# Optimization experiments

Hardware: AMD Instinct MI355X
Metric: run time of the kernel (lower is better)

## Reference

```python
import jax, jax.numpy as jnp
import numpy as np

NUM_HEADS = 32
HEAD_DIM = 32  # hard-coded in the module


def _rope_sincos(seq_len, head_dim):
    # NOTE: module uses arange(0, head_dim)/head_dim (full dim, not the usual /2 stride)
    inv_freq = 1.0 / (10000.0 ** (jnp.arange(0, head_dim, dtype=jnp.float32) / head_dim))
    freqs = jnp.outer(jnp.arange(seq_len, dtype=jnp.float32), inv_freq)  # [S, D]
    # original repeats over heads then reshapes -> identical values per head,
    # so broadcasting with shape [1, S, 1, D] is equivalent.
    return jnp.sin(freqs)[None, :, None, :], jnp.cos(freqs)[None, :, None, :]


def _apply_rope(x, sin, cos):
    x1, x2 = jnp.split(x, 2, axis=-1)
    x_rot = jnp.concatenate([-x2, x1], axis=-1)
    return x * cos + x_rot * sin


def setup_inputs() -> dict:
    key = jax.random.key(0)
    B, S, H, D = 2, 2048, NUM_HEADS, HEAD_DIM
    dm = H * D
    k1, k2 = jax.random.split(key)
    x = jax.random.normal(k1, (B, S, dm), dtype=jnp.float32)
    W_qkv = jax.random.normal(k2, (dm, 3 * dm), dtype=jnp.float32) / np.sqrt(dm).astype(np.float32)
    mask = jnp.tril(jnp.ones((S, S), dtype=bool))[None, None]  # causal, [1,1,S,S]
    return {"x": x, "W_qkv": W_qkv, "mask": mask}


def reference(x, W_qkv, mask):
    B, S, dm = x.shape
    H, D = NUM_HEADS, HEAD_DIM
    qkv = x @ W_qkv  # [B, S, 3*H*D], no bias
    q, k, v = jnp.split(qkv, 3, axis=-1)
    q = q.reshape(B, S, H, D)
    k = k.reshape(B, S, H, D)
    v = v.reshape(B, S, H, D)

    sin, cos = _rope_sincos(S, D)
    q = _apply_rope(q, sin, cos)
    k = _apply_rope(k, sin, cos)

    # [B, H, S, D]
    q = q.transpose(0, 2, 1, 3)
    k = k.transpose(0, 2, 1, 3)
    v = v.transpose(0, 2, 1, 3)

    scale = 1.0 / np.sqrt(D).astype(np.float32)
    attn = jnp.einsum('bhqd,bhkd->bhqk', q, k) * scale  # [B, H, S, S]
    attn = jnp.where(mask, attn, jnp.float32(-jnp.inf))
    attn = jax.nn.softmax(attn, axis=-1)
    out = jnp.einsum('bhqk,bhkd->bhqd', attn, v)  # [B, H, S, D]
    return out.transpose(0, 2, 1, 3).reshape(B, S, H * D)
```

## Files before the change

kernel.cpp:

```cpp
#include <hip/hip_runtime.h>
#include <cstdint>
#include <cstddef>

#define BB 2
#define SS 2048
#define HH 32
#define DD 32
#define DM 1024
#define MROWS 4096
#define NQKV 3072

#define QSCALE 0.25503486f

typedef __attribute__((ext_vector_type(8))) short bf16x8;
typedef __attribute__((ext_vector_type(4))) float f32x4;
typedef __attribute__((address_space(1))) unsigned int gu32;
typedef __attribute__((address_space(3))) unsigned int lu32;

__device__ __forceinline__ unsigned short f2bf(float f) {
    union { float f; unsigned int u; } v;
    v.f = f;
    unsigned int u = v.u;
    u += 0x7fffu + ((u >> 16) & 1u);
    return (unsigned short)(u >> 16);
}

__device__ __forceinline__ unsigned int cvt_pk_bf16(float a, float b) {
    unsigned int r;
    asm("v_cvt_pk_bf16_f32 %0, %1, %2" : "=v"(r) : "v"(a), "v"(b));
    return r;
}

__global__ void conv_x_k(const float* __restrict__ x, unsigned short* __restrict__ xb, int n4) {
    int i = blockIdx.x * 256 + threadIdx.x;
    if (i < n4) {
        float4 v = ((const float4*)x)[i];
        ushort4 o;
        o.x = f2bf(v.x); o.y = f2bf(v.y); o.z = f2bf(v.z); o.w = f2bf(v.w);
        ((ushort4*)xb)[i] = o;
    }
}

__global__ void conv_wT_k(const float* __restrict__ w, unsigned short* __restrict__ wT) {
    __shared__ unsigned short tile[64][65];
    const int n0 = blockIdx.x * 64;
    const int k0 = blockIdx.y * 64;
    const int tx = threadIdx.x & 63;
    const int ty = threadIdx.x >> 6;
    for (int i = ty; i < 64; i += 4)
        tile[i][tx] = f2bf(w[(size_t)(k0 + i) * NQKV + n0 + tx]);
    __syncthreads();
    for (int i = ty; i < 64; i += 4)
        wT[(size_t)(n0 + i) * 1024 + k0 + tx] = tile[tx][i];
}

__global__ void rope_tab_k(float* __restrict__ st, float* __restrict__ ct) {
    int i = blockIdx.x * 256 + threadIdx.x;
    int s = i >> 5, d = i & 31;
    float inv = exp2f((float)d * -0.41524101186092029f);
    float f = (float)s * inv;
    float sv, cv;
    sincosf(f, &sv, &cv);
    st[i] = sv;
    ct[i] = cv;
}

__global__ __launch_bounds__(256) void qkv_gemm_k(
        const unsigned short* __restrict__ xb,
        const unsigned short* __restrict__ wTp,
        const float* __restrict__ st, const float* __restrict__ ct,
        unsigned short* __restrict__ qbuf,
        unsigned short* __restrict__ kbuf,
        unsigned short* __restrict__ vtbuf) {
    __shared__ unsigned short smem[2 * 128 * 32];
    unsigned short* As = smem;
    unsigned short* Bs = smem + 4096;
    const int m0 = blockIdx.x * 128;
    const int n0 = blockIdx.y * 128;
    const int tid = threadIdx.x;
    const int w = tid >> 6, lane = tid & 63;
    const int quad = lane >> 4, l16 = lane & 15;
    const int wr = w >> 1, wc = w & 1;

    f32x4 acc[4][4];
#pragma unroll
    for (int i = 0; i < 4; ++i)
#pragma unroll
        for (int j = 0; j < 4; ++j)
            acc[i][j] = (f32x4){0.f, 0.f, 0.f, 0.f};

    const int Ra = lane >> 2;
    const int ca = lane & 3;

    for (int k0 = 0; k0 < 1024; k0 += 32) {
        __syncthreads();
#pragma unroll
        for (int q = 0; q < 2; ++q) {
            const int seg = w * 2 + q;
            const int row = seg * 16 + Ra;
            const unsigned short* ga = xb  + (size_t)(m0 + row) * 1024 + k0 + ca * 8;
            const unsigned short* gb = wTp + (size_t)(n0 + row) * 1024 + k0 + ca * 8;
            __builtin_amdgcn_global_load_lds((gu32*)ga, (lu32*)(As + seg * 512), 16, 0, 0);
            __builtin_amdgcn_global_load_lds((gu32*)gb, (lu32*)(Bs + seg * 512), 16, 0, 0);
        }
        __syncthreads();
        bf16x8 af[4], bfv[4];
#pragma unroll
        for (int i = 0; i < 4; ++i)
            af[i] = *(const bf16x8*)(As + (wr * 64 + i * 16 + l16) * 32 + quad * 8);
#pragma unroll
        for (int j = 0; j < 4; ++j)
            bfv[j] = *(const bf16x8*)(Bs + (wc * 64 + j * 16 + l16) * 32 + quad * 8);
#pragma unroll
        for (int i = 0; i < 4; ++i)
#pragma unroll
            for (int j = 0; j < 4; ++j)
                acc[i][j] = __builtin_amdgcn_mfma_f32_16x16x32_bf16(af[i], bfv[j], acc[i][j], 0, 0, 0);
    }

    const int sec = n0 >> 10;
    const int rowb = m0 + wr * 64;
    const int colb = n0 + wc * 64;
    if (sec < 2) {
        unsigned short* dst = (sec == 0) ? qbuf : kbuf;
        const float qs = (sec == 0) ? QSCALE : 1.0f;
        const int d1 = l16, d2 = l16 + 16;
#pragma unroll
        for (int jp = 0; jp < 2; ++jp) {
            const int col1 = colb + jp * 32 + l16;
            const int h = (col1 & 1023) >> 5;
#pragma unroll
            for (int i = 0; i < 4; ++i) {
#pragma unroll
                for (int r = 0; r < 4; ++r) {
                    const int row = rowb + i * 16 + quad * 4 + r;
                    const int bb = row >> 11;
                    const int s = row & 2047;
                    const float x1 = acc[i][jp * 2][r];
                    const float x2 = acc[i][jp * 2 + 1][r];
                    const float sn1 = st[s * 32 + d1] * qs, cs1 = ct[s * 32 + d1] * qs;
                    const float sn2 = st[s * 32 + d2] * qs, cs2 = ct[s * 32 + d2] * qs;
                    unsigned short o1 = f2bf(x1 * cs1 - x2 * sn1);
                    unsigned short o2 = f2bf(x2 * cs2 + x1 * sn2);
                    unsigned short* p = dst + (size_t)((bb * 32 + h) * 2048 + s) * 32;
                    p[d1] = o1;
                    p[d2] = o2;
                }
            }
        }
    } else {
        __syncthreads();
        unsigned short* tw = smem + w * 2048;
        const int bbi = rowb >> 11;
        const int srow = rowb & 2047;
        const int colB = colb - 2048;
#pragma unroll
        for (int j = 0; j < 4; ++j) {
#pragma unroll
            for (int i = 0; i < 4; ++i) {
                uint2 pk;
                pk.x = cvt_pk_bf16(acc[i][j][0], acc[i][j][1]);
                pk.y = cvt_pk_bf16(acc[i][j][2], acc[i][j][3]);
                *(uint2*)&tw[l16 * 66 + i * 16 + quad * 4] = pk;
            }
#pragma unroll
            for (int c = 0; c < 16; ++c) {
                const int col = colB + j * 16 + c;
                const int hh = col >> 5, d = col & 31;
                vtbuf[((size_t)(bbi * 32 + hh) * 32 + d) * 2048 + srow + lane] = tw[c * 66 + lane];
            }
        }
    }
}

__global__ __launch_bounds__(256) void attn_k(
        const unsigned short* __restrict__ qb,
        const unsigned short* __restrict__ kb,
        const unsigned short* __restrict__ vt,
        float* __restrict__ out) {
    __shared__ unsigned short Pl[4][2][32][40];
    const int tid = threadIdx.x;
    const int w = tid >> 6, lane = tid & 63;
    const int quad = lane >> 4, l16 = lane & 15;
    const int bh = blockIdx.x >> 3;
    const int pr = blockIdx.x & 7;
    const int b = bh >> 5, h = bh & 31;

    const unsigned short* qbase = qb + (size_t)bh * 2048 * 32;
    const unsigned short* kbase = kb + (size_t)bh * 2048 * 32;
    const unsigned short* vbase = vt + (size_t)bh * 32 * 2048;
    const f32x4 fz = {0.f, 0.f, 0.f, 0.f};

    for (int ph = 0; ph < 2; ++ph) {
        const int qw = (ph == 0) ? (pr * 128 + w * 32)
                                 : ((15 - pr) * 128 + (3 - w) * 32);
        const int nkt = (qw >> 5) + 1;

        bf16x8 qf0 = *(const bf16x8*)(qbase + (size_t)(qw + l16) * 32 + quad * 8);
        bf16x8 qf1 = *(const bf16x8*)(qbase + (size_t)(qw + 16 + l16) * 32 + quad * 8);

        f32x4 a00 = fz, a01 = fz, a10 = fz, a11 = fz;
        float ls0 = 0.f, ls1 = 0.f;

        const unsigned short* kp0 = kbase + (size_t)l16 * 32 + quad * 8;
        const unsigned short* kp1 = kbase + (size_t)(16 + l16) * 32 + quad * 8;
        const unsigned short* vp0 = vbase + (size_t)l16 * 2048 + quad * 8;
        const unsigned short* vp1 = vbase + (size_t)(16 + l16) * 2048 + quad * 8;

        bf16x8 kc0 = *(const bf16x8*)kp0;
        bf16x8 kc1 = *(const bf16x8*)kp1;
        bf16x8 vc0 = *(const bf16x8*)vp0;
        bf16x8 vc1 = *(const bf16x8*)vp1;

        for (int kt = 0; kt < nkt - 1; ++kt) {
            kp0 += 1024; kp1 += 1024; vp0 += 32; vp1 += 32;
            bf16x8 kn0 = *(const bf16x8*)kp0;
            bf16x8 kn1 = *(const bf16x8*)kp1;
            bf16x8 vn0 = *(const bf16x8*)vp0;
            bf16x8 vn1 = *(const bf16x8*)vp1;

            f32x4 s00 = __builtin_amdgcn_mfma_f32_16x16x32_bf16(kc0, qf0, fz, 0, 0, 0);
            f32x4 s01 = __builtin_amdgcn_mfma_f32_16x16x32_bf16(kc0, qf1, fz, 0, 0, 0);
            f32x4 s10 = __builtin_amdgcn_mfma_f32_16x16x32_bf16(kc1, qf0, fz, 0, 0, 0);
            f32x4 s11 = __builtin_amdgcn_mfma_f32_16x16x32_bf16(kc1, qf1, fz, 0, 0, 0);

            unsigned short (*plw)[40] = Pl[w][kt & 1];
            {
                float p0 = __builtin_amdgcn_exp2f(s00[0]), p1 = __builtin_amdgcn_exp2f(s00[1]);
                float p2 = __builtin_amdgcn_exp2f(s00[2]), p3 = __builtin_amdgcn_exp2f(s00[3]);
                ls0 += (p0 + p1) + (p2 + p3);
                uint2 pk; pk.x = cvt_pk_bf16(p0, p1); pk.y = cvt_pk_bf16(p2, p3);
                *(uint2*)&plw[l16][quad * 4] = pk;
            }
            {
                float p0 = __builtin_amdgcn_exp2f(s01[0]), p1 = __builtin_amdgcn_exp2f(s01[1]);
                float p2 = __builtin_amdgcn_exp2f(s01[2]), p3 = __builtin_amdgcn_exp2f(s01[3]);
                ls1 += (p0 + p1) + (p2 + p3);
                uint2 pk; pk.x = cvt_pk_bf16(p0, p1); pk.y = cvt_pk_bf16(p2, p3);
                *(uint2*)&plw[16 + l16][quad * 4] = pk;
            }
            {
                float p0 = __builtin_amdgcn_exp2f(s10[0]), p1 = __builtin_amdgcn_exp2f(s10[1]);
                float p2 = __builtin_amdgcn_exp2f(s10[2]), p3 = __builtin_amdgcn_exp2f(s10[3]);
                ls0 += (p0 + p1) + (p2 + p3);
                uint2 pk; pk.x = cvt_pk_bf16(p0, p1); pk.y = cvt_pk_bf16(p2, p3);
                *(uint2*)&plw[l16][16 + quad * 4] = pk;
            }
            {
                float p0 = __builtin_amdgcn_exp2f(s11[0]), p1 = __builtin_amdgcn_exp2f(s11[1]);
                float p2 = __builtin_amdgcn_exp2f(s11[2]), p3 = __builtin_amdgcn_exp2f(s11[3]);
                ls1 += (p0 + p1) + (p2 + p3);
                uint2 pk; pk.x = cvt_pk_bf16(p0, p1); pk.y = cvt_pk_bf16(p2, p3);
                *(uint2*)&plw[16 + l16][16 + quad * 4] = pk;
            }

            bf16x8 pf0 = *(const bf16x8*)&plw[l16][quad * 8];
            bf16x8 pf1 = *(const bf16x8*)&plw[16 + l16][quad * 8];
            a00 = __builtin_amdgcn_mfma_f32_16x16x32_bf16(vc0, pf0, a00, 0, 0, 0);
            a01 = __builtin_amdgcn_mfma_f32_16x16x32_bf16(vc0, pf1, a01, 0, 0, 0);
            a10 = __builtin_amdgcn_mfma_f32_16x16x32_bf16(vc1, pf0, a10, 0, 0, 0);
            a11 = __builtin_amdgcn_mfma_f32_16x16x32_bf16(vc1, pf1, a11, 0, 0, 0);

            kc0 = kn0; kc1 = kn1; vc0 = vn0; vc1 = vn1;
        }

        {
            f32x4 s00 = __builtin_amdgcn_mfma_f32_16x16x32_bf16(kc0, qf0, fz, 0, 0, 0);
            f32x4 s01 = __builtin_amdgcn_mfma_f32_16x16x32_bf16(kc0, qf1, fz, 0, 0, 0);
            f32x4 s11 = __builtin_amdgcn_mfma_f32_16x16x32_bf16(kc1, qf1, fz, 0, 0, 0);

            unsigned short (*plw)[40] = Pl[w][(nkt - 1) & 1];
            {
                float p[4];
#pragma unroll
                for (int r = 0; r < 4; ++r)
                    p[r] = (quad * 4 + r > l16) ? 0.f : __builtin_amdgcn_exp2f(s00[r]);
                ls0 += (p[0] + p[1]) + (p[2] + p[3]);
                uint2 pk; pk.x = cvt_pk_bf16(p[0], p[1]); pk.y = cvt_pk_bf16(p[2], p[3]);
                *(uint2*)&plw[l16][quad * 4] = pk;
            }
            {
                float p0 = __builtin_amdgcn_exp2f(s01[0]), p1 = __builtin_amdgcn_exp2f(s01[1]);
                float p2 = __builtin_amdgcn_exp2f(s01[2]), p3 = __builtin_amdgcn_exp2f(s01[3]);
                ls1 += (p0 + p1) + (p2 + p3);
                uint2 pk; pk.x = cvt_pk_bf16(p0, p1); pk.y = cvt_pk_bf16(p2, p3);
                *(uint2*)&plw[16 + l16][quad * 4] = pk;
            }
            {
                uint2 pk; pk.x = 0; pk.y = 0;
                *(uint2*)&plw[l16][16 + quad * 4] = pk;
            }
            {
                float p[4];
#pragma unroll
                for (int r = 0; r < 4; ++r)
                    p[r] = (quad * 4 + r > l16) ? 0.f : __builtin_amdgcn_exp2f(s11[r]);
                ls1 += (p[0] + p[1]) + (p[2] + p[3]);
                uint2 pk; pk.x = cvt_pk_bf16(p[0], p[1]); pk.y = cvt_pk_bf16(p[2], p[3]);
                *(uint2*)&plw[16 + l16][16 + quad * 4] = pk;
            }

            bf16x8 pf0 = *(const bf16x8*)&plw[l16][quad * 8];
            bf16x8 pf1 = *(const bf16x8*)&plw[16 + l16][quad * 8];
            a00 = __builtin_amdgcn_mfma_f32_16x16x32_bf16(vc0, pf0, a00, 0, 0, 0);
            a01 = __builtin_amdgcn_mfma_f32_16x16x32_bf16(vc0, pf1, a01, 0, 0, 0);
            a10 = __builtin_amdgcn_mfma_f32_16x16x32_bf16(vc1, pf0, a10, 0, 0, 0);
            a11 = __builtin_amdgcn_mfma_f32_16x16x32_bf16(vc1, pf1, a11, 0, 0, 0);
        }

        float l0 = ls0; l0 += __shfl_xor(l0, 16); l0 += __shfl_xor(l0, 32);
        float l1 = ls1; l1 += __shfl_xor(l1, 16); l1 += __shfl_xor(l1, 32);
        const float inv0 = 1.f / l0, inv1 = 1.f / l1;

        float* ot = (float*)&Pl[w][0][0][0];
        {
            f32x4 t;
            t = a00; t[0]*=inv0; t[1]*=inv0; t[2]*=inv0; t[3]*=inv0;
            *(f32x4*)&ot[(l16) * 36 + quad * 4] = t;
            t = a10; t[0]*=inv0; t[1]*=inv0; t[2]*=inv0; t[3]*=inv0;
            *(f32x4*)&ot[(l16) * 36 + 16 + quad * 4] = t;
            t = a01; t[0]*=inv1; t[1]*=inv1; t[2]*=inv1; t[3]*=inv1;
            *(f32x4*)&ot[(16 + l16) * 36 + quad * 4] = t;
            t = a11; t[0]*=inv1; t[1]*=inv1; t[2]*=inv1; t[3]*=inv1;
            *(f32x4*)&ot[(16 + l16) * 36 + 16 + quad * 4] = t;
        }
        const int dd = lane & 31, qpar = lane >> 5;
        float* ob = out + (size_t)(b * 2048 + qw) * 1024 + h * 32;
#pragma unroll
        for (int i2 = 0; i2 < 16; ++i2) {
            const int qloc = i2 * 2 + qpar;
            ob[(size_t)qloc * 1024 + dd] = ot[qloc * 36 + dd];
        }
    }
}

extern "C" void kernel_launch(void* const* d_in, const int* in_sizes, int n_in,
                              void* d_out, int out_size, void* d_ws, size_t ws_size,
                              hipStream_t stream) {
    (void)in_sizes; (void)n_in; (void)out_size; (void)ws_size;
    const float* x = (const float*)d_in[0];
    const float* wq = (const float*)d_in[1];
    float* out = (float*)d_out;

    unsigned short* xb = (unsigned short*)d_ws;
    unsigned short* wT = xb + (size_t)MROWS * DM;
    unsigned short* qb = wT + (size_t)NQKV * DM;
    unsigned short* kb = qb + (size_t)BB * HH * SS * DD;
    unsigned short* vt = kb + (size_t)BB * HH * SS * DD;
    float* st = (float*)(vt + (size_t)BB * HH * SS * DD);
    float* ct = st + (size_t)SS * DD;

    conv_x_k<<<dim3(MROWS * DM / 4 / 256), dim3(256), 0, stream>>>(x, xb, MROWS * DM / 4);
    conv_wT_k<<<dim3(NQKV / 64, DM / 64), dim3(256), 0, stream>>>(wq, wT);
    rope_tab_k<<<dim3(SS * DD / 256), dim3(256), 0, stream>>>(st, ct);
    qkv_gemm_k<<<dim3(MROWS / 128, NQKV / 128), dim3(256), 0, stream>>>(xb, wT, st, ct, qb, kb, vt);
    attn_k<<<dim3(BB * HH * 8), dim3(256), 0, stream>>>(qb, kb, vt, out);
}
```

Before: 187.2 us.

## Fuse prep kernels, swizzle GEMM LDS tiles, vectorize RoPE epilogue table loads

Merges the three preprocessing kernels (x conversion, weight transpose, RoPE table) into one launch by partitioning the block index. The GEMM's LDS layout gains an XOR swizzle on both the global_load_lds source addressing and the fragment reads, to reduce bank conflicts. The RoPE epilogue reads one packed float4 (sin/cos for d and d+16), with the Q scale prebaked into a separate table, instead of four scalar loads and multiplies. It also uses the hardware bf16 pack conversion. Saves launch overhead and epilogue memory traffic, at the cost of a more intricate address mapping.

Result: faster. 181.2 us (-3.2%).

```diff
diff --git a/kernel.cpp b/kernel.cpp
--- a/kernel.cpp
+++ b/kernel.cpp
@@ -30,45 +30,53 @@
     asm("v_cvt_pk_bf16_f32 %0, %1, %2" : "=v"(r) : "v"(a), "v"(b));
     return r;
 }
-
-__global__ void conv_x_k(const float* __restrict__ x, unsigned short* __restrict__ xb, int n4) {
-    int i = blockIdx.x * 256 + threadIdx.x;
-    if (i < n4) {
+__device__ __forceinline__ unsigned short bf1(float a) {
+    return (unsigned short)cvt_pk_bf16(a, a);
+}
+
+__global__ __launch_bounds__(256) void prep_k(
+        const float* __restrict__ x, const float* __restrict__ w,
+        unsigned short* __restrict__ xb, unsigned short* __restrict__ wT,
+        float* __restrict__ tk, float* __restrict__ tq) {
+    __shared__ unsigned short tile[64][65];
+    const int blk = blockIdx.x;
+    const int tid = threadIdx.x;
+    if (blk < 4096) {
+        const int i = blk * 256 + tid;
         float4 v = ((const float4*)x)[i];
         ushort4 o;
         o.x = f2bf(v.x); o.y = f2bf(v.y); o.z = f2bf(v.z); o.w = f2bf(v.w);
         ((ushort4*)xb)[i] = o;
+    } else if (blk < 4864) {
+        const int bx = blk - 4096;
+        const int n0 = (bx % 48) * 64;
+        const int k0 = (bx / 48) * 64;
+        const int tx = tid & 63;
+        const int ty = tid >> 6;
+        for (int i = ty; i < 64; i += 4)
+            tile[i][tx] = f2bf(w[(size_t)(k0 + i) * NQKV + n0 + tx]);
+        __syncthreads();
+        for (int i = ty; i < 64; i += 4)
+            wT[(size_t)(n0 + i) * 1024 + k0 + tx] = tile[tx][i];
+    } else {
+        const int i = (blk - 4864) * 256 + tid;
+        const int s = i >> 4, dl = i & 15;
+        const float inv1 = exp2f((float)dl * -0.41524101186092029f);
+        const float inv2 = exp2f((float)(dl + 16) * -0.41524101186092029f);
+        float s1, c1, s2, c2;
+        sincosf((float)s * inv1, &s1, &c1);
+        sincosf((float)s * inv2, &s2, &c2);
+        float4 vk = {s1, c1, s2, c2};
+        float4 vq = {s1 * QSCALE, c1 * QSCALE, s2 * QSCALE, c2 * QSCALE};
+        ((float4*)tk)[i] = vk;
+        ((float4*)tq)[i] = vq;
     }
-}
-
-__global__ void conv_wT_k(const float* __restrict__ w, unsigned short* __restrict__ wT) {
-    __shared__ unsigned short tile[64][65];
-    const int n0 = blockIdx.x * 64;
-    const int k0 = blockIdx.y * 64;
-    const int tx = threadIdx.x & 63;
-    const int ty = threadIdx.x >> 6;
-    for (int i = ty; i < 64; i += 4)
-        tile[i][tx] = f2bf(w[(size_t)(k0 + i) * NQKV + n0 + tx]);
-    __syncthreads();
-    for (int i = ty; i < 64; i += 4)
-        wT[(size_t)(n0 + i) * 1024 + k0 + tx] = tile[tx][i];
-}
-
-__global__ void rope_tab_k(float* __restrict__ st, float* __restrict__ ct) {
-    int i = blockIdx.x * 256 + threadIdx.x;
-    int s = i >> 5, d = i & 31;
-    float inv = exp2f((float)d * -0.41524101186092029f);
-    float f = (float)s * inv;
-    float sv, cv;
-    sincosf(f, &sv, &cv);
-    st[i] = sv;
-    ct[i] = cv;
 }
 
 __global__ __launch_bounds__(256) void qkv_gemm_k(
         const unsigned short* __restrict__ xb,
         const unsigned short* __restrict__ wTp,
-        const float* __restrict__ st, const float* __restrict__ ct,
+        const float4* __restrict__ tk, const float4* __restrict__ tq,
         unsigned short* __restrict__ qbuf,
         unsigned short* __restrict__ kbuf,
         unsigned short* __restrict__ vtbuf) {
@@ -89,17 +97,19 @@
         for (int j = 0; j < 4; ++j)
             acc[i][j] = (f32x4){0.f, 0.f, 0.f, 0.f};
 
-    const int Ra = lane >> 2;
-    const int ca = lane & 3;
+    const int G = (lane & 56) | ((lane ^ (lane >> 3)) & 7);
+    const int goff = (G >> 2) * 1024 + (G & 3) * 8;
+    const int Gr = l16 * 4 + quad;
+    const int L = Gr ^ ((Gr >> 3) & 7);
+    const int roff = L * 8;
 
     for (int k0 = 0; k0 < 1024; k0 += 32) {
         __syncthreads();
 #pragma unroll
         for (int q = 0; q < 2; ++q) {
             const int seg = w * 2 + q;
-            const int row = seg * 16 + Ra;
-            const unsigned short* ga = xb  + (size_t)(m0 + row) * 1024 + k0 + ca * 8;
-            const unsigned short* gb = wTp + (size_t)(n0 + row) * 1024 + k0 + ca * 8;
+            const unsigned short* ga = xb  + (size_t)(m0 + seg * 16) * 1024 + k0 + goff;
+            const unsigned short* gb = wTp + (size_t)(n0 + seg * 16) * 1024 + k0 + goff;
             __builtin_amdgcn_global_load_lds((gu32*)ga, (lu32*)(As + seg * 512), 16, 0, 0);
             __builtin_amdgcn_global_load_lds((gu32*)gb, (lu32*)(Bs + seg * 512), 16, 0, 0);
         }
@@ -107,10 +117,10 @@
         bf16x8 af[4], bfv[4];
 #pragma unroll
         for (int i = 0; i < 4; ++i)
-            af[i] = *(const bf16x8*)(As + (wr * 64 + i * 16 + l16) * 32 + quad * 8);
+            af[i] = *(const bf16x8*)(As + (wr * 4 + i) * 512 + roff);
 #pragma unroll
         for (int j = 0; j < 4; ++j)
-            bfv[j] = *(const bf16x8*)(Bs + (wc * 64 + j * 16 + l16) * 32 + quad * 8);
+            bfv[j] = *(const bf16x8*)(Bs + (wc * 4 + j) * 512 + roff);
 #pragma unroll
         for (int i = 0; i < 4; ++i)
 #pragma unroll
@@ -123,28 +133,28 @@
     const int colb = n0 + wc * 64;
     if (sec < 2) {
         unsigned short* dst = (sec == 0) ? qbuf : kbuf;
-        const float qs = (sec == 0) ? QSCALE : 1.0f;
-        const int d1 = l16, d2 = l16 + 16;
-#pragma unroll
-        for (int jp = 0; jp < 2; ++jp) {
-            const int col1 = colb + jp * 32 + l16;
-            const int h = (col1 & 1023) >> 5;
-#pragma unroll
-            for (int i = 0; i < 4; ++i) {
-#pragma unroll
-                for (int r = 0; r < 4; ++r) {
-                    const int row = rowb + i * 16 + quad * 4 + r;
-                    const int bb = row >> 11;
-                    const int s = row & 2047;
-                    const float x1 = acc[i][jp * 2][r];
-                    const float x2 = acc[i][jp * 2 + 1][r];
-                    const float sn1 = st[s * 32 + d1] * qs, cs1 = ct[s * 32 + d1] * qs;
-                    const float sn2 = st[s * 32 + d2] * qs, cs2 = ct[s * 32 + d2] * qs;
-                    unsigned short o1 = f2bf(x1 * cs1 - x2 * sn1);
-                    unsigned short o2 = f2bf(x2 * cs2 + x1 * sn2);
-                    unsigned short* p = dst + (size_t)((bb * 32 + h) * 2048 + s) * 32;
-                    p[d1] = o1;
-                    p[d2] = o2;
+        const float4* tab = (sec == 0) ? tq : tk;
+        const int h0 = (colb & 1023) >> 5;
+        const int h1 = ((colb + 32) & 1023) >> 5;
+#pragma unroll
+        for (int i = 0; i < 4; ++i) {
+#pragma unroll
+            for (int r = 0; r < 4; ++r) {
+                const int row = rowb + i * 16 + quad * 4 + r;
+                const int bb = row >> 11, s = row & 2047;
+                const float4 t = tab[s * 16 + l16];
+                unsigned short* pb = dst + ((size_t)(bb * 32) * 2048 + s) * 32;
+                {
+                    const float x1 = acc[i][0][r], x2 = acc[i][1][r];
+                    unsigned short* p = pb + (size_t)h0 * (2048 * 32);
+                    p[l16]      = bf1(x1 * t.y - x2 * t.x);
+                    p[l16 + 16] = bf1(x2 * t.w + x1 * t.z);
+                }
+                {
+                    const float x1 = acc[i][2][r], x2 = acc[i][3][r];
+                    unsigned short* p = pb + (size_t)h1 * (2048 * 32);
+                    p[l16]      = bf1(x1 * t.y - x2 * t.x);
+                    p[l16 + 16] = bf1(x2 * t.w + x1 * t.z);
                 }
             }
         }
@@ -347,12 +357,11 @@
     unsigned short* qb = wT + (size_t)NQKV * DM;
     unsigned short* kb = qb + (size_t)BB * HH * SS * DD;
     unsigned short* vt = kb + (size_t)BB * HH * SS * DD;
-    float* st = (float*)(vt + (size_t)BB * HH * SS * DD);
-    float* ct = st + (size_t)SS * DD;
-
-    conv_x_k<<<dim3(MROWS * DM / 4 / 256), dim3(256), 0, stream>>>(x, xb, MROWS * DM / 4);
-    conv_wT_k<<<dim3(NQKV / 64, DM / 64), dim3(256), 0, stream>>>(wq, wT);
-    rope_tab_k<<<dim3(SS * DD / 256), dim3(256), 0, stream>>>(st, ct);
-    qkv_gemm_k<<<dim3(MROWS / 128, NQKV / 128), dim3(256), 0, stream>>>(xb, wT, st, ct, qb, kb, vt);
+    float* tk = (float*)(vt + (size_t)BB * HH * SS * DD);
+    float* tq = tk + (size_t)SS * 16 * 4;
+
+    prep_k<<<dim3(4992), dim3(256), 0, stream>>>(x, wq, xb, wT, tk, tq);
+    qkv_gemm_k<<<dim3(MROWS / 128, NQKV / 128), dim3(256), 0, stream>>>(
+        xb, wT, (const float4*)tk, (const float4*)tq, qb, kb, vt);
     attn_k<<<dim3(BB * HH * 8), dim3(256), 0, stream>>>(qb, kb, vt, out);
 }
```
